# Optimization experiments

Hardware: AMD Instinct MI355X
Metric: run time of the kernel (lower is better)

## Reference

```python
import jax, jax.numpy as jnp
import numpy as np

N, M, C, T, H, W = 32, 20, 512, 4, 7, 7  # batch, max_others, channels, t, h, w
L = 4  # temp_pos_len
STD = 0.01


def setup_inputs() -> dict:
    key = jax.random.key(0)
    ks = jax.random.split(key, 12)
    return {
        "person": jax.random.normal(ks[0], (N, C, T, H, W), jnp.float32),
        "others": jax.random.normal(ks[1], (N, M, C, T, H, W), jnp.float32),
        "Wq": jax.random.normal(ks[2], (C, C), jnp.float32) * STD,
        "bq": jax.random.normal(ks[3], (C,), jnp.float32) * STD,
        "Wk": jax.random.normal(ks[4], (C, C), jnp.float32) * STD,
        "bk": jax.random.normal(ks[5], (C,), jnp.float32) * STD,
        "Wv": jax.random.normal(ks[6], (C, C), jnp.float32) * STD,
        "bv": jax.random.normal(ks[7], (C,), jnp.float32) * STD,
        "Wo": jax.random.normal(ks[8], (C, C), jnp.float32) * STD,
        "bo": jax.random.normal(ks[9], (C,), jnp.float32) * STD,
        "pos_k": jax.random.normal(ks[10], (L, C), jnp.float32) * 0.02,
        "pos_v": jax.random.normal(ks[11], (L, C), jnp.float32) * 0.02,
    }


def reference(person, others, Wq, bq, Wk, bk, Wv, bv, Wo, bo, pos_k, pos_v):
    n, c, t, h, w = person.shape
    _, m, _, to, ho, wo = others.shape
    scale = c ** (-0.5)

    # 1x1x1 conv projections == channel matmuls
    q = jnp.einsum('oc,ncthw->nothw', Wq, person) + bq[None, :, None, None, None]
    k = jnp.einsum('oc,nmcthw->nmothw', Wk, others) + bk[None, None, :, None, None, None]
    v = jnp.einsum('oc,nmcthw->nmothw', Wv, others) + bv[None, None, :, None, None, None]

    # additive temporal positional bias on K/V: others split into L temporal groups
    Lp = pos_k.shape[0]
    P = m // Lp  # max_person_per_sec
    k = (k.reshape(n, Lp, P, c, to, ho, wo)
         + pos_k[None, :, None, :, None, None, None]).reshape(n, m, c, to, ho, wo)
    v = (v.reshape(n, Lp, P, c, to, ho, wo)
         + pos_v[None, :, None, :, None, None, None]).reshape(n, m, c, to, ho, wo)

    S = t * h * w          # query length
    K = m * to * ho * wo   # key length
    qf = q.reshape(n, c, S).transpose(0, 2, 1)                              # [n,S,c]
    kf = k.reshape(n, m, c, to * ho * wo).transpose(0, 1, 3, 2).reshape(n, K, c)
    vf = v.reshape(n, m, c, to * ho * wo).transpose(0, 1, 3, 2).reshape(n, K, c)

    attn = jax.nn.softmax(jnp.einsum('nsc,nkc->nsk', qf, kf) * scale, axis=-1)
    o = jnp.einsum('nsk,nkc->nsc', attn, vf)                                # [n,S,c]
    o = o.transpose(0, 2, 1).reshape(n, c, t, h, w)

    # LayerNorm over [c,t,h,w] per sample, no affine
    mu = jnp.mean(o, axis=(1, 2, 3, 4), keepdims=True)
    var = jnp.var(o, axis=(1, 2, 3, 4), keepdims=True)
    o = (o - mu) * jax.lax.rsqrt(var + 1e-5)

    o = jax.nn.relu(o)
    o = jnp.einsum('oc,ncthw->nothw', Wo, o) + bo[None, :, None, None, None]
    return o + person  # shortcut is identity (dim_person == dim_out)
```

## Files before the change

### kernel.cpp

```cpp
#include <hip/hip_runtime.h>
#include <hip/hip_bf16.h>

#define N_B 32
#define M_O 20
#define C_C 512
#define S_S 196
#define S_P 208
#define K_K 3920
#define K_P 4096
#define SCALEF 0.044194173824159216f

typedef short s4v __attribute__((ext_vector_type(4)));
typedef short s8v __attribute__((ext_vector_type(8)));
typedef float f4v __attribute__((ext_vector_type(4)));

__device__ __forceinline__ f4v mfma16(s8v a, s8v b, f4v c){
  return __builtin_amdgcn_mfma_f32_16x16x32_bf16(a, b, c, 0, 0, 0);
}
__device__ __forceinline__ unsigned short f2b(float x){
  __hip_bfloat16 h = __float2bfloat16(x);
  return *reinterpret_cast<unsigned short*>(&h);
}
__device__ __forceinline__ float b2f(short u){
  unsigned int v = ((unsigned int)(unsigned short)u) << 16;
  return __uint_as_float(v);
}

#define GLOAD16(g, l) __builtin_amdgcn_global_load_lds( \
    (const __attribute__((address_space(1))) unsigned int*)(g), \
    (__attribute__((address_space(3))) unsigned int*)(l), 16, 0, 0)

__global__ void k_sentinel(float* out, float v){ out[threadIdx.x] = v; }

__global__ void k_cvt(const float* __restrict__ w0, const float* __restrict__ w1,
                      const float* __restrict__ w2, const float* __restrict__ w3,
                      unsigned short* __restrict__ out){
  int i = blockIdx.x*256 + threadIdx.x;
  int m = i >> 16;
  int r = i & 65535;
  const float* s = (m==0)?w0:((m==1)?w1:((m==2)?w2:w3));
  f4v v = ((const f4v*)s)[r];
  s4v o = { (short)f2b(v[0]), (short)f2b(v[1]), (short)f2b(v[2]), (short)f2b(v[3]) };
  ((s4v*)out)[i] = o;
}

__global__ __launch_bounds__(256) void k_tr(const float* __restrict__ X,
                                            unsigned short* __restrict__ Xt){
  const int cc = blockIdx.x * 64;
  const int slab = blockIdx.y;
  const int tid = threadIdx.x;
  __shared__ unsigned short A[196][72];
  const int row = tid >> 2;
  const int j   = tid & 3;
  const float* src = X + (size_t)slab*(C_C*S_S) + (size_t)(cc+row)*S_S;
  for (int p = j; p < 49; p += 4){
    f4v v = *(const f4v*)(src + p*4);
    int s = p*4;
    A[s+0][row] = f2b(v[0]);
    A[s+1][row] = f2b(v[1]);
    A[s+2][row] = f2b(v[2]);
    A[s+3][row] = f2b(v[3]);
  }
  __syncthreads();
  unsigned short* dst = Xt + (size_t)slab*(S_S*C_C) + cc;
  for (int v = tid; v < S_S*8; v += 256){
    int s = v >> 3, c8 = v & 7;
    *(s8v*)(dst + (size_t)s*C_C + c8*8) = *(const s8v*)&A[s][c8*8];
  }
}

template<bool HASV>
__global__ __launch_bounds__(256, 2) void k_projgemm(
    const unsigned short* __restrict__ Xt,
    const unsigned short* __restrict__ W1, const float* __restrict__ b1, const float* __restrict__ pos1,
    const unsigned short* __restrict__ W2, const float* __restrict__ b2, const float* __restrict__ pos2,
    unsigned short* __restrict__ outK, unsigned short* __restrict__ outVT)
{
  const int id = blockIdx.x;
  const int work = HASV ? ((id & 7)*980 + (id >> 3)) : id;
  const int ct    = HASV ? (work & 3) : (work & 1);
  const int rtile = HASV ? (work >> 2) : (work >> 1);
  const int r0 = rtile*64;
  const int cb = ct * (HASV ? 128 : 256);
  const int tid = threadIdx.x, wid = tid>>6, lane = tid&63;
  const int lr = lane&15, lq = lane>>4;
  const int mat = wid >> 1, chalf = (wid & 1)*64;
  const bool isV = HASV && (mat == 1);

  const unsigned short* WB = HASV ? W2 : W1;
  const int cbB = HASV ? cb : cb + 128;

  __shared__ unsigned short SA[2][2][2048];
  __shared__ unsigned short SB[2][2][8192];

  f4v acc[4][4];
  #pragma unroll
  for (int i=0;i<4;i++)
    #pragma unroll
    for (int j=0;j<4;j++) acc[i][j]=(f4v){0,0,0,0};

  const int rsub = lane >> 2;
  const int csub = ((lane & 3) ^ ((rsub>>1)&3)) * 8;

  auto STAGE = [&](int buf, int h, int c0){
    const unsigned short* ga = Xt + (size_t)(r0 + wid*16 + rsub)*C_C + c0 + h*32 + csub;
    GLOAD16(ga, &SA[buf][h][(wid*16)*32]);
    #pragma unroll
    for (int j=0;j<4;j++){
      const int br = j*64 + wid*16 + rsub;
      const unsigned short* gw = (j<2)
        ? W1 + (size_t)(cb  + br      )*C_C + c0 + h*32 + csub
        : WB + (size_t)(cbB + br - 128)*C_C + c0 + h*32 + csub;
      GLOAD16(gw, &SB[buf][h][(j*64 + wid*16)*32]);
    }
  };

  STAGE(0, 0, 0);
  STAGE(0, 1, 0);
  asm volatile("s_waitcnt vmcnt(5)" ::: "memory");
  __builtin_amdgcn_s_barrier();

  const int bbase = mat*128 + chalf;
  const int rchunk = (lq ^ ((lr>>1)&3)) * 8;
  for (int it = 0; it < 8; ++it){
    const int buf = it & 1;
    #pragma unroll
    for (int h = 0; h < 2; ++h){
      s8v af[4], bf[4];
      #pragma unroll
      for (int i=0;i<4;i++)
        af[i] = *(const s8v*)&SA[buf][h][(i*16 + lr)*32 + rchunk];
      #pragma unroll
      for (int i=0;i<4;i++)
        bf[i] = *(const s8v*)&SB[buf][h][(bbase + i*16 + lr)*32 + rchunk];
      if (it < 7){
        STAGE(buf^1, h, (it+1)*64);
        asm volatile("s_waitcnt vmcnt(5)" ::: "memory");
      } else {
        asm volatile("s_waitcnt vmcnt(0)" ::: "memory");
      }
      __builtin_amdgcn_s_barrier();
      asm volatile("s_waitcnt lgkmcnt(0)" ::: "memory");
      __builtin_amdgcn_sched_barrier(0);
      __builtin_amdgcn_s_setprio(1);
      if (!isV){
        #pragma unroll
        for (int ot=0;ot<4;ot++)
          #pragma unroll
          for (int rt=0;rt<4;rt++)
            acc[rt][ot] = mfma16(af[rt], bf[ot], acc[rt][ot]);
      } else {
        #pragma unroll
        for (int ot=0;ot<4;ot++)
          #pragma unroll
          for (int rt=0;rt<4;rt++)
            acc[ot][rt] = mfma16(bf[ot], af[rt], acc[ot][rt]);
      }
      __builtin_amdgcn_s_setprio(0);
      __builtin_amdgcn_s_barrier();
    }
  }

  const int cout = HASV ? (cb + chalf) : (cb + mat*128 + chalf);
  if (!isV){
    #pragma unroll
    for (int ot=0;ot<4;ot++){
      const int o = cout + ot*16 + lr;
      const float bb = b1[o];
      #pragma unroll
      for (int rt=0;rt<4;rt++){
        #pragma unroll
        for (int rr=0;rr<4;rr++){
          const int r = r0 + rt*16 + lq*4 + rr;
          float bias = bb;
          if (HASV) bias += pos1[((r % K_K)/980)*C_C + o];
          outK[(size_t)r*C_C + o] = f2b(acc[rt][ot][rr] + bias);
        }
      }
    }
  } else {
    #pragma unroll
    for (int ot=0;ot<4;ot++){
      #pragma unroll
      for (int rr=0;rr<4;rr++){
        const int o = cout + ot*16 + lq*4 + rr;
        const float bb = b2[o];
        #pragma unroll
        for (int rt=0;rt<4;rt++){
          const int r = r0 + rt*16 + lr;
          const int n = r / K_K;
          const int rn = r - n*K_K;
          const float bias = bb + pos2[(rn/980)*C_C + o];
          outVT[(size_t)n*C_C*K_P + (size_t)o*K_P + rn] = f2b(acc[ot][rt][rr] + bias);
        }
      }
    }
  }
}

__global__ __launch_bounds__(512, 2) void k_scores(
    const unsigned short* __restrict__ A, const unsigned short* __restrict__ B,
    unsigned short* __restrict__ out16, float* __restrict__ rowsum)
{
  const int tid = threadIdx.x, wid = tid>>6, lane = tid&63;
  const int lr = lane&15, lq = lane>>4;
  const int wr = wid>>2, wc = wid&3;

  int x = blockIdx.x & 7, idx = blockIdx.x >> 3;
  int w = x*128 + idx;
  const int nslab = w >> 5; int sub = w & 31;
  const int ctsel = sub & 15, rtile = sub >> 4;
  const int r0 = rtile*128;
  const unsigned short* Aslab = A + (size_t)nslab*S_S*C_C;
  const unsigned short* Bslab = B + (size_t)nslab*K_K*C_C + (size_t)ctsel*256*512;

  __shared__ unsigned short SA[2][4096];
  __shared__ unsigned short SB[2][8192];

  f4v acc[4][4];
  #pragma unroll
  for (int i=0;i<4;i++)
    #pragma unroll
    for (int j=0;j<4;j++) acc[i][j]=(f4v){0,0,0,0};

  const int rsub = lane >> 2;
  const int csub = ((lane & 3) ^ ((rsub>>1)&3)) * 8;

  auto STAGE = [&](int buf, int c0){
    GLOAD16(Aslab + (size_t)(r0 + wid*16 + rsub)*512 + c0 + csub,
            &SA[buf][(wid*16)*32]);
    GLOAD16(Bslab + (size_t)(wid*16 + rsub)*512 + c0 + csub,
            &SB[buf][(wid*16)*32]);
    GLOAD16(Bslab + (size_t)(128 + wid*16 + rsub)*512 + c0 + csub,
            &SB[buf][(128 + wid*16)*32]);
  };

  STAGE(0, 0);

  const int rchunk = (lq ^ ((lr>>1)&3)) * 8;
  for (int it = 0; it < 16; ++it){
    const int buf = it & 1;
    if (it < 15){
      STAGE(buf^1, (it+1)*32);
      asm volatile("s_waitcnt vmcnt(3)" ::: "memory");
    } else {
      asm volatile("s_waitcnt vmcnt(0)" ::: "memory");
    }
    __builtin_amdgcn_s_barrier();
    s8v af[4], bf[4];
    #pragma unroll
    for (int i=0;i<4;i++)
      af[i] = *(const s8v*)&SA[buf][(wr*64 + i*16 + lr)*32 + rchunk];
    #pragma unroll
    for (int j=0;j<4;j++)
      bf[j] = *(const s8v*)&SB[buf][(wc*64 + j*16 + lr)*32 + rchunk];
    #pragma unroll
    for (int ot=0;ot<4;ot++)
      #pragma unroll
      for (int rt=0;rt<4;rt++)
        acc[rt][ot] = mfma16(af[rt], bf[ot], acc[rt][ot]);
    __builtin_amdgcn_s_barrier();
  }

  float psum[4][4];
  #pragma unroll
  for (int rt=0;rt<4;rt++)
    #pragma unroll
    for (int rr=0;rr<4;rr++) psum[rt][rr] = 0.f;

  #pragma unroll
  for (int ot=0;ot<4;ot++){
    const int kcol = ctsel*256 + wc*64 + ot*16 + lr;
    #pragma unroll
    for (int rt=0;rt<4;rt++){
      #pragma unroll
      for (int rr=0;rr<4;rr++){
        const int s = r0 + wr*64 + rt*16 + lq*4 + rr;
        float e = (kcol < K_K) ? __expf(acc[rt][ot][rr]*SCALEF) : 0.f;
        psum[rt][rr] += e;
        if (s < S_P)
          out16[((size_t)nslab*S_P + s)*K_P + kcol] = f2b(e);
      }
    }
  }
  #pragma unroll
  for (int rt=0;rt<4;rt++){
    #pragma unroll
    for (int rr=0;rr<4;rr++){
      float v = psum[rt][rr];
      v += __shfl_xor(v, 1);
      v += __shfl_xor(v, 2);
      v += __shfl_xor(v, 4);
      v += __shfl_xor(v, 8);
      if (lr == 0){
        const int s = r0 + wr*64 + rt*16 + lq*4 + rr;
        if (s < S_P) atomicAdd(&rowsum[nslab*S_P + s], v);
      }
    }
  }
}

__global__ __launch_bounds__(256, 2) void k_pv(
    const unsigned short* __restrict__ A, const unsigned short* __restrict__ B,
    const float* __restrict__ rowsum, float* __restrict__ out32)
{
  const int tid = threadIdx.x, wid = tid>>6, lane = tid&63;
  const int lr = lane&15, lq = lane>>4;
  const int wr = wid>>1, wc = wid&1;

  int x = blockIdx.x & 7, idx = blockIdx.x >> 3;
  int w = x*64 + idx;
  const int nslab = w >> 4; int sub = w & 15;
  const int ks = sub >> 3, rtile = (sub>>2)&1, ctsel = sub & 3;
  const int r0 = rtile*128;
  const int koff = ks*2048;
  const unsigned short* Aslab = A + (size_t)nslab*S_P*K_P;
  const unsigned short* Bslab = B + (size_t)nslab*C_C*K_P + (size_t)ctsel*128*K_P;

  __shared__ unsigned short SA[2][4096];
  __shared__ unsigned short SB[2][4096];

  f4v acc[4][4];
  #pragma unroll
  for (int i=0;i<4;i++)
    #pragma unroll
    for (int j=0;j<4;j++) acc[i][j]=(f4v){0,0,0,0};

  const int rsub = lane >> 2;
  const int csub = ((lane & 3) ^ ((rsub>>1)&3)) * 8;

  auto STAGE = [&](int buf, int c0){
    GLOAD16(Aslab + (size_t)(r0 + wid*16 + rsub)*K_P + c0 + csub,
            &SA[buf][(wid*16)*32]);
    GLOAD16(Aslab + (size_t)(r0 + 64 + wid*16 + rsub)*K_P + c0 + csub,
            &SA[buf][(64 + wid*16)*32]);
    GLOAD16(Bslab + (size_t)(wid*16 + rsub)*K_P + c0 + csub,
            &SB[buf][(wid*16)*32]);
    GLOAD16(Bslab + (size_t)(64 + wid*16 + rsub)*K_P + c0 + csub,
            &SB[buf][(64 + wid*16)*32]);
  };

  STAGE(0, koff);

  const int rchunk = (lq ^ ((lr>>1)&3)) * 8;
  for (int it = 0; it < 64; ++it){
    const int buf = it & 1;
    if (it < 63){
      STAGE(buf^1, koff + (it+1)*32);
      asm volatile("s_waitcnt vmcnt(4)" ::: "memory");
    } else {
      asm volatile("s_waitcnt vmcnt(0)" ::: "memory");
    }
    __builtin_amdgcn_s_barrier();
    s8v af[4], bf[4];
    #pragma unroll
    for (int i=0;i<4;i++)
      af[i] = *(const s8v*)&SA[buf][(wr*64 + i*16 + lr)*32 + rchunk];
    #pragma unroll
    for (int j=0;j<4;j++)
      bf[j] = *(const s8v*)&SB[buf][(wc*64 + j*16 + lr)*32 + rchunk];
    #pragma unroll
    for (int ot=0;ot<4;ot++)
      #pragma unroll
      for (int rt=0;rt<4;rt++)
        acc[rt][ot] = mfma16(af[rt], bf[ot], acc[rt][ot]);
    __builtin_amdgcn_s_barrier();
  }

  float invs[4][4];
  #pragma unroll
  for (int rt=0;rt<4;rt++){
    #pragma unroll
    for (int rr=0;rr<4;rr++){
      const int s = r0 + wr*64 + rt*16 + lq*4 + rr;
      invs[rt][rr] = (s < S_P) ? 1.f/rowsum[(size_t)nslab*S_P + s] : 0.f;
    }
  }
  float* op = out32 + (size_t)ks*(N_B*S_P*C_C);
  #pragma unroll
  for (int ot=0;ot<4;ot++){
    const int c = ctsel*128 + wc*64 + ot*16 + lr;
    #pragma unroll
    for (int rt=0;rt<4;rt++){
      #pragma unroll
      for (int rr=0;rr<4;rr++){
        const int s = r0 + wr*64 + rt*16 + lq*4 + rr;
        if (s < S_P)
          op[((size_t)nslab*S_P + s)*C_C + c] = acc[rt][ot][rr]*invs[rt][rr];
      }
    }
  }
}

__global__ void k_lnpart(const float* __restrict__ O0, const float* __restrict__ O1,
                         float* __restrict__ sums){
  const int part = blockIdx.x, n = blockIdx.y;
  const int tid = threadIdx.x;
  const size_t base = ((size_t)n*S_P + part*49)*C_C;
  float ls=0.f, ls2=0.f;
  for (int i = tid; i < 49*C_C/4; i += 256){
    f4v a = ((const f4v*)(O0+base))[i];
    f4v b = ((const f4v*)(O1+base))[i];
    #pragma unroll
    for (int j=0;j<4;j++){ float v = a[j]+b[j]; ls += v; ls2 += v*v; }
  }
  #pragma unroll
  for (int d=32;d>=1;d>>=1){ ls += __shfl_xor(ls,d); ls2 += __shfl_xor(ls2,d); }
  __shared__ float r1[4], r2[4];
  if ((tid&63)==0){ r1[tid>>6]=ls; r2[tid>>6]=ls2; }
  __syncthreads();
  if (tid==0){
    atomicAdd(&sums[n*2],   r1[0]+r1[1]+r1[2]+r1[3]);
    atomicAdd(&sums[n*2+1], r2[0]+r2[1]+r2[2]+r2[3]);
  }
}

__global__ void k_norm(const float* __restrict__ O0, const float* __restrict__ O1,
                       const float* __restrict__ sums, unsigned short* __restrict__ ob){
  size_t g = (size_t)blockIdx.x*256 + threadIdx.x;
  int n = (int)(g / (S_P*C_C/8));
  int rem = (int)(g - (size_t)n*(S_P*C_C/8));
  int s = rem / (C_C/8);
  const float inv = 1.f/((float)S_S*C_C);
  float mu = sums[n*2]*inv;
  float var = sums[n*2+1]*inv - mu*mu;
  float rq = rsqrtf(var + 1e-5f);
  const f4v* s0 = (const f4v*)(O0 + g*8);
  const f4v* s1 = (const f4v*)(O1 + g*8);
  f4v a0 = s0[0], a1 = s0[1], b0 = s1[0], b1 = s1[1];
  unsigned short o16[8];
  if (s < S_S){
    #pragma unroll
    for (int i=0;i<4;i++){ float y=(a0[i]+b0[i]-mu)*rq; o16[i]=f2b(fmaxf(y,0.f)); }
    #pragma unroll
    for (int i=0;i<4;i++){ float y=(a1[i]+b1[i]-mu)*rq; o16[4+i]=f2b(fmaxf(y,0.f)); }
  } else {
    #pragma unroll
    for (int i=0;i<8;i++) o16[i]=0;
  }
  *(s8v*)(ob + g*8) = *(const s8v*)o16;
}

__global__ __launch_bounds__(256) void k_final(const unsigned short* __restrict__ ob,
    const unsigned short* __restrict__ Wo, const float* __restrict__ bo,
    const float* __restrict__ person, float* __restrict__ out)
{
  const int ocb = blockIdx.x, n = blockIdx.y;
  const int tid=threadIdx.x, wid=tid>>6, lane=tid&63, lr=lane&15, lq=lane>>4;
  const int ocb0 = ocb*64 + wid*16;
  const unsigned short* obp = ob + (size_t)n*S_P*C_C;
  f4v acc[13];
  #pragma unroll
  for (int i=0;i<13;i++) acc[i]=(f4v){0,0,0,0};
  for (int c0=0;c0<C_C;c0+=32){
    s8v af = *(const s8v*)(Wo + (size_t)(ocb0+lr)*C_C + c0 + lq*8);
    #pragma unroll
    for (int ct=0;ct<13;ct++){
      s8v bfv = *(const s8v*)(obp + (size_t)(ct*16+lr)*C_C + c0 + lq*8);
      acc[ct]=mfma16(af,bfv,acc[ct]);
    }
  }
  #pragma unroll
  for (int ct=0;ct<13;ct++){
    #pragma unroll
    for (int r=0;r<4;r++){
      int oc = ocb0 + lq*4 + r;
      int s = ct*16 + lr;
      if (s < S_S){
        size_t idx = ((size_t)n*C_C + oc)*S_S + s;
        out[idx] = acc[ct][r] + bo[oc] + person[idx];
      }
    }
  }
}

extern "C" void kernel_launch(void* const* d_in, const int* in_sizes, int n_in,
                              void* d_out, int out_size, void* d_ws, size_t ws_size,
                              hipStream_t stream)
{
  (void)in_sizes; (void)n_in; (void)out_size;
  const float* person = (const float*)d_in[0];
  const float* others = (const float*)d_in[1];
  const float* Wq = (const float*)d_in[2];
  const float* bq = (const float*)d_in[3];
  const float* Wk = (const float*)d_in[4];
  const float* bk = (const float*)d_in[5];
  const float* Wv = (const float*)d_in[6];
  const float* bv = (const float*)d_in[7];
  const float* Wo = (const float*)d_in[8];
  const float* bo = (const float*)d_in[9];
  const float* pos_k = (const float*)d_in[10];
  const float* pos_v = (const float*)d_in[11];
  float* out = (float*)d_out;

  char* ws = (char*)d_ws;
  size_t off = 0;
  auto alloc = [&](size_t bytes)->char*{
    char* p = ws + off; off += (bytes + 255) & ~(size_t)255; return p;
  };
  unsigned short* Wb  = (unsigned short*)alloc(4ull*C_C*C_C*2);
  unsigned short* Xt  = (unsigned short*)alloc(((size_t)N_B*M_O*S_S + 16)*C_C*2);
  unsigned short* Qt  = (unsigned short*)alloc(((size_t)N_B*S_S + 16)*C_C*2);
  unsigned short* qb  = (unsigned short*)alloc(((size_t)N_B*S_S + 64)*C_C*2);
  unsigned short* kfb = (unsigned short*)alloc(((size_t)N_B*K_K + 256)*C_C*2);
  unsigned short* vtb = (unsigned short*)alloc((size_t)N_B*C_C*K_P*2);
  unsigned short* Sbuf= (unsigned short*)alloc(((size_t)N_B*S_P + 64)*K_P*2);
  float* sums         = (float*)alloc(2*N_B*sizeof(float));
  float* rowsum       = (float*)alloc((size_t)N_B*S_P*sizeof(float));

  float* Obuf         = (float*)Xt;
  unsigned short* obb = (unsigned short*)((char*)Xt +
                          ((2ull*N_B*S_P*C_C*4 + 255) & ~(size_t)255));

  if (off > ws_size) {
    k_sentinel<<<1,256,0,stream>>>(out, (float)(ws_size>>20));
    return;
  }

  unsigned short* Wq_b = Wb;
  unsigned short* Wk_b = Wb + 262144;
  unsigned short* Wv_b = Wb + 2*262144;
  unsigned short* Wo_b = Wb + 3*262144;
  float* O1 = Obuf + (size_t)N_B*S_P*C_C;

  hipMemsetAsync(sums, 0, 2*N_B*sizeof(float), stream);
  hipMemsetAsync(rowsum, 0, (size_t)N_B*S_P*sizeof(float), stream);
  k_cvt<<<1024,256,0,stream>>>(Wq,Wk,Wv,Wo,Wb);
  k_tr<<<dim3(8,N_B*M_O),256,0,stream>>>(others, Xt);
  k_tr<<<dim3(8,N_B),256,0,stream>>>(person, Qt);
  k_projgemm<true ><<<7840,256,0,stream>>>(Xt,
      Wk_b, bk, pos_k, Wv_b, bv, pos_v, kfb, vtb);
  k_projgemm<false><<<196,256,0,stream>>>(Qt,
      Wq_b, bq, nullptr, nullptr, nullptr, nullptr, qb, nullptr);
  k_scores<<<1024,512,0,stream>>>(qb, kfb, Sbuf, rowsum);
  k_pv<<<512,256,0,stream>>>(Sbuf, vtb, rowsum, Obuf);
  k_lnpart<<<dim3(4,N_B),256,0,stream>>>(Obuf, O1, sums);
  k_norm<<<1664,256,0,stream>>>(Obuf, O1, sums, obb);
  k_final<<<dim3(8,N_B),256,0,stream>>>(obb, Wo_b, bo, person, out);
}
```

Before: 571.6 us.

## Deepen GEMM K-pipelining with 64-wide double-buffered halves and MFMA priority

Both the scores and PV GEMM kernels now stage 64 channels per outer step, split into two 32-wide halves in double-buffered LDS. Each half's LDS fragment reads are issued before the next global prefetch and barrier. The MFMA block runs under raised wave priority behind a scheduling fence. The aim is to overlap global loads, LDS reads and MFMA work and to reduce stalls per barrier. LDS use doubles, which may lower occupancy against the 2-blocks-per-CU launch bounds, and the per-half barrier count stays the same.

After: 602.9 us. +5.5%, slower.

```diff
diff --git a/kernel.cpp b/kernel.cpp
--- a/kernel.cpp
+++ b/kernel.cpp
@@ -214,8 +214,8 @@
   const unsigned short* Aslab = A + (size_t)nslab*S_S*C_C;
   const unsigned short* Bslab = B + (size_t)nslab*K_K*C_C + (size_t)ctsel*256*512;
 
-  __shared__ unsigned short SA[2][4096];
-  __shared__ unsigned short SB[2][8192];
+  __shared__ unsigned short SA[2][2][4096];
+  __shared__ unsigned short SB[2][2][8192];
 
   f4v acc[4][4];
   #pragma unroll
@@ -226,40 +226,50 @@
   const int rsub = lane >> 2;
   const int csub = ((lane & 3) ^ ((rsub>>1)&3)) * 8;
 
-  auto STAGE = [&](int buf, int c0){
-    GLOAD16(Aslab + (size_t)(r0 + wid*16 + rsub)*512 + c0 + csub,
-            &SA[buf][(wid*16)*32]);
-    GLOAD16(Bslab + (size_t)(wid*16 + rsub)*512 + c0 + csub,
-            &SB[buf][(wid*16)*32]);
-    GLOAD16(Bslab + (size_t)(128 + wid*16 + rsub)*512 + c0 + csub,
-            &SB[buf][(128 + wid*16)*32]);
+  auto STAGE = [&](int buf, int h, int c0){
+    GLOAD16(Aslab + (size_t)(r0 + wid*16 + rsub)*512 + c0 + h*32 + csub,
+            &SA[buf][h][(wid*16)*32]);
+    GLOAD16(Bslab + (size_t)(wid*16 + rsub)*512 + c0 + h*32 + csub,
+            &SB[buf][h][(wid*16)*32]);
+    GLOAD16(Bslab + (size_t)(128 + wid*16 + rsub)*512 + c0 + h*32 + csub,
+            &SB[buf][h][(128 + wid*16)*32]);
   };
 
-  STAGE(0, 0);
+  STAGE(0, 0, 0);
+  STAGE(0, 1, 0);
+  asm volatile("s_waitcnt vmcnt(3)" ::: "memory");
+  __builtin_amdgcn_s_barrier();
 
   const int rchunk = (lq ^ ((lr>>1)&3)) * 8;
-  for (int it = 0; it < 16; ++it){
+  for (int it = 0; it < 8; ++it){
     const int buf = it & 1;
-    if (it < 15){
-      STAGE(buf^1, (it+1)*32);
-      asm volatile("s_waitcnt vmcnt(3)" ::: "memory");
-    } else {
-      asm volatile("s_waitcnt vmcnt(0)" ::: "memory");
-    }
-    __builtin_amdgcn_s_barrier();
-    s8v af[4], bf[4];
-    #pragma unroll
-    for (int i=0;i<4;i++)
-      af[i] = *(const s8v*)&SA[buf][(wr*64 + i*16 + lr)*32 + rchunk];
-    #pragma unroll
-    for (int j=0;j<4;j++)
-      bf[j] = *(const s8v*)&SB[buf][(wc*64 + j*16 + lr)*32 + rchunk];
-    #pragma unroll
-    for (int ot=0;ot<4;ot++)
-      #pragma unroll
-      for (int rt=0;rt<4;rt++)
-        acc[rt][ot] = mfma16(af[rt], bf[ot], acc[rt][ot]);
-    __builtin_amdgcn_s_barrier();
+    #pragma unroll
+    for (int h = 0; h < 2; ++h){
+      s8v af[4], bf[4];
+      #pragma unroll
+      for (int i=0;i<4;i++)
+        af[i] = *(const s8v*)&SA[buf][h][(wr*64 + i*16 + lr)*32 + rchunk];
+      #pragma unroll
+      for (int j=0;j<4;j++)
+        bf[j] = *(const s8v*)&SB[buf][h][(wc*64 + j*16 + lr)*32 + rchunk];
+      if (it < 7){
+        STAGE(buf^1, h, (it+1)*64);
+        asm volatile("s_waitcnt vmcnt(3)" ::: "memory");
+      } else {
+        asm volatile("s_waitcnt vmcnt(0)" ::: "memory");
+      }
+      __builtin_amdgcn_s_barrier();
+      asm volatile("s_waitcnt lgkmcnt(0)" ::: "memory");
+      __builtin_amdgcn_sched_barrier(0);
+      __builtin_amdgcn_s_setprio(1);
+      #pragma unroll
+      for (int ot=0;ot<4;ot++)
+        #pragma unroll
+        for (int rt=0;rt<4;rt++)
+          acc[rt][ot] = mfma16(af[rt], bf[ot], acc[rt][ot]);
+      __builtin_amdgcn_s_setprio(0);
+      __builtin_amdgcn_s_barrier();
+    }
   }
 
   float psum[4][4];
@@ -317,8 +327,8 @@
   const unsigned short* Aslab = A + (size_t)nslab*S_P*K_P;
   const unsigned short* Bslab = B + (size_t)nslab*C_C*K_P + (size_t)ctsel*128*K_P;
 
-  __shared__ unsigned short SA[2][4096];
-  __shared__ unsigned short SB[2][4096];
+  __shared__ unsigned short SA[2][2][4096];
+  __shared__ unsigned short SB[2][2][4096];
 
   f4v acc[4][4];
   #pragma unroll
@@ -329,42 +339,53 @@
   const int rsub = lane >> 2;
   const int csub = ((lane & 3) ^ ((rsub>>1)&3)) * 8;
 
-  auto STAGE = [&](int buf, int c0){
-    GLOAD16(Aslab + (size_t)(r0 + wid*16 + rsub)*K_P + c0 + csub,
-            &SA[buf][(wid*16)*32]);
-    GLOAD16(Aslab + (size_t)(r0 + 64 + wid*16 + rsub)*K_P + c0 + csub,
-            &SA[buf][(64 + wid*16)*32]);
-    GLOAD16(Bslab + (size_t)(wid*16 + rsub)*K_P + c0 + csub,
-            &SB[buf][(wid*16)*32]);
-    GLOAD16(Bslab + (size_t)(64 + wid*16 + rsub)*K_P + c0 + csub,
-            &SB[buf][(64 + wid*16)*32]);
+  auto STAGE = [&](int buf, int h, int c0){
+    const int cc = c0 + h*32;
+    GLOAD16(Aslab + (size_t)(r0 + wid*16 + rsub)*K_P + cc + csub,
+            &SA[buf][h][(wid*16)*32]);
+    GLOAD16(Aslab + (size_t)(r0 + 64 + wid*16 + rsub)*K_P + cc + csub,
+            &SA[buf][h][(64 + wid*16)*32]);
+    GLOAD16(Bslab + (size_t)(wid*16 + rsub)*K_P + cc + csub,
+            &SB[buf][h][(wid*16)*32]);
+    GLOAD16(Bslab + (size_t)(64 + wid*16 + rsub)*K_P + cc + csub,
+            &SB[buf][h][(64 + wid*16)*32]);
   };
 
-  STAGE(0, koff);
+  STAGE(0, 0, koff);
+  STAGE(0, 1, koff);
+  asm volatile("s_waitcnt vmcnt(4)" ::: "memory");
+  __builtin_amdgcn_s_barrier();
 
   const int rchunk = (lq ^ ((lr>>1)&3)) * 8;
-  for (int it = 0; it < 64; ++it){
+  for (int it = 0; it < 32; ++it){
     const int buf = it & 1;
-    if (it < 63){
-      STAGE(buf^1, koff + (it+1)*32);
-      asm volatile("s_waitcnt vmcnt(4)" ::: "memory");
-    } else {
-      asm volatile("s_waitcnt vmcnt(0)" ::: "memory");
-    }
-    __builtin_amdgcn_s_barrier();
-    s8v af[4], bf[4];
-    #pragma unroll
-    for (int i=0;i<4;i++)
-      af[i] = *(const s8v*)&SA[buf][(wr*64 + i*16 + lr)*32 + rchunk];
-    #pragma unroll
-    for (int j=0;j<4;j++)
-      bf[j] = *(const s8v*)&SB[buf][(wc*64 + j*16 + lr)*32 + rchunk];
-    #pragma unroll
-    for (int ot=0;ot<4;ot++)
-      #pragma unroll
-      for (int rt=0;rt<4;rt++)
-        acc[rt][ot] = mfma16(af[rt], bf[ot], acc[rt][ot]);
-    __builtin_amdgcn_s_barrier();
+    #pragma unroll
+    for (int h = 0; h < 2; ++h){
+      s8v af[4], bf[4];
+      #pragma unroll
+      for (int i=0;i<4;i++)
+        af[i] = *(const s8v*)&SA[buf][h][(wr*64 + i*16 + lr)*32 + rchunk];
+      #pragma unroll
+      for (int j=0;j<4;j++)
+        bf[j] = *(const s8v*)&SB[buf][h][(wc*64 + j*16 + lr)*32 + rchunk];
+      if (it < 31){
+        STAGE(buf^1, h, koff + (it+1)*64);
+        asm volatile("s_waitcnt vmcnt(4)" ::: "memory");
+      } else {
+        asm volatile("s_waitcnt vmcnt(0)" ::: "memory");
+      }
+      __builtin_amdgcn_s_barrier();
+      asm volatile("s_waitcnt lgkmcnt(0)" ::: "memory");
+      __builtin_amdgcn_sched_barrier(0);
+      __builtin_amdgcn_s_setprio(1);
+      #pragma unroll
+      for (int ot=0;ot<4;ot++)
+        #pragma unroll
+        for (int rt=0;rt<4;rt++)
+          acc[rt][ot] = mfma16(af[rt], bf[ot], acc[rt][ot]);
+      __builtin_amdgcn_s_setprio(0);
+      __builtin_amdgcn_s_barrier();
+    }
   }
 
   float invs[4][4];
```
